# Kernel tuning notes

Measured on AMD Instinct MI355X. Metric: run time of the kernel, lower is better.

## Reference

```python
import jax, jax.numpy as jnp
import numpy as np

B, L, T = 8, 4096, 128
D_H, D_G, D_PROJ = 1024, 256, 256


def setup_inputs() -> dict:
    key = jax.random.key(0)
    k1, k2, k3, k4, k5 = jax.random.split(key, 5)
    H = jax.random.normal(k1, (B, L, D_H), dtype=jnp.float32)
    G = jax.random.normal(k2, (B, T, D_G), dtype=jnp.float32)
    mask = jax.random.randint(k3, (B, L), 0, 2) == 1  # True = masked out
    Wk = jax.random.normal(k4, (D_H, D_PROJ), dtype=jnp.float32) * 0.02
    Wq = jax.random.normal(k5, (D_G, D_PROJ), dtype=jnp.float32) * 0.02
    return {"H": H, "G": G, "mask": mask, "Wk": Wk, "Wq": Wq}


def reference(H, G, mask, Wk, Wq):
    scale = D_PROJ ** (-0.5)
    K = jnp.einsum('bld,dp->blp', H, Wk)          # [B, L, d_proj]
    Q = jnp.einsum('btd,dp->btp', G, Wq)          # [B, T, d_proj]
    logits = jnp.einsum('btp,blp->btl', Q, K) * scale  # [B, T, L]
    logits = jnp.where(mask[:, None, :], -jnp.inf, logits)
    alpha = jax.nn.softmax(logits, axis=-1)       # [B, T, L]
    Z = jnp.einsum('btl,bld->btd', alpha, H)      # [B, T, d_h]
    return Z
```

## Files before the change

kernel.cpp:

```cpp
#include <hip/hip_runtime.h>
#include <hip/hip_bf16.h>
#include <math.h>

#define B_  8
#define L_  4096
#define T_  128
#define DH  1024
#define DG  256
#define DP  256
#define BK  64
#define ZCH 8

typedef short bf16x8 __attribute__((ext_vector_type(8)));
typedef float f32x4  __attribute__((ext_vector_type(4)));
typedef unsigned short u16x8 __attribute__((ext_vector_type(8)));

#define AS1(p) ((const __attribute__((address_space(1))) void*)(p))
#define AS3(p) ((__attribute__((address_space(3))) void*)(p))

#define SYNC() do { asm volatile("s_waitcnt lgkmcnt(0)" ::: "memory"); \
                    __builtin_amdgcn_s_barrier(); \
                    __builtin_amdgcn_sched_barrier(0); } while (0)

__device__ __forceinline__ unsigned short f2bf(float f) {
    unsigned u = __float_as_uint(f);
    unsigned r = (u + 0x7FFFu + ((u >> 16) & 1u)) >> 16;
    return (unsigned short)r;
}

__device__ __forceinline__ char* swz(void* base, int row, int colbytes) {
    return (char*)base + (((row << 7) + colbytes) ^ ((row & 7) << 4));
}
__device__ __forceinline__ const char* swzc(const void* base, int row, int colbytes) {
    return (const char*)base + (((row << 7) + colbytes) ^ ((row & 7) << 4));
}

__global__ __launch_bounds__(256) void wct_kernel(const float* __restrict__ Wk,
                                                  const float* __restrict__ Wq,
                                                  unsigned short* __restrict__ Wct) {
    __shared__ __attribute__((aligned(16))) unsigned short As[128 * BK];
    __shared__ __attribute__((aligned(16))) unsigned short Bs[64 * BK];
    const int n0 = blockIdx.x * 64, m0 = blockIdx.y * 128;
    const int tid = threadIdx.x, wave = tid >> 6, lane = tid & 63;
    const int lm = lane & 15, quad = lane >> 4;
    const int wm = wave >> 1, wn = wave & 1;
    const int bc = (tid & 15) * 4, br = tid >> 4;
    f32x4 acc[4][2] = {};

    for (int k0 = 0; k0 < DP; k0 += BK) {
        #pragma unroll
        for (int s = 0; s < 8; ++s) {
            const int row = br + s * 16;
            const float4 v = *(const float4*)(Wk + (size_t)(m0 + row) * DP + k0 + bc);
            ushort4 p; p.x = f2bf(v.x); p.y = f2bf(v.y); p.z = f2bf(v.z); p.w = f2bf(v.w);
            *(ushort4*)(&As[row * BK + bc]) = p;
        }
        #pragma unroll
        for (int s = 0; s < 4; ++s) {
            const int row = br + s * 16;
            const float4 v = *(const float4*)(Wq + (size_t)(n0 + row) * DP + k0 + bc);
            ushort4 p; p.x = f2bf(v.x); p.y = f2bf(v.y); p.z = f2bf(v.z); p.w = f2bf(v.w);
            *(ushort4*)(&Bs[row * BK + bc]) = p;
        }
        __syncthreads();
        #pragma unroll
        for (int ks = 0; ks < 2; ++ks) {
            bf16x8 a[4], bf[2];
            #pragma unroll
            for (int i = 0; i < 4; ++i)
                a[i] = *(const bf16x8*)(&As[(wm * 64 + i * 16 + lm) * BK + ks * 32 + quad * 8]);
            #pragma unroll
            for (int j = 0; j < 2; ++j)
                bf[j] = *(const bf16x8*)(&Bs[(wn * 32 + j * 16 + lm) * BK + ks * 32 + quad * 8]);
            #pragma unroll
            for (int i = 0; i < 4; ++i)
                #pragma unroll
                for (int j = 0; j < 2; ++j)
                    acc[i][j] = __builtin_amdgcn_mfma_f32_16x16x32_bf16(a[i], bf[j], acc[i][j], 0, 0, 0);
        }
        __syncthreads();
    }
    unsigned short* Cb = Wct + (size_t)m0 * DG + n0;
    #pragma unroll
    for (int i = 0; i < 4; ++i)
        #pragma unroll
        for (int j = 0; j < 2; ++j)
            #pragma unroll
            for (int r = 0; r < 4; ++r)
                Cb[(size_t)(wm * 64 + i * 16 + quad * 4 + r) * DG + wn * 32 + j * 16 + lm] =
                    f2bf(acc[i][j][r] * 0.0625f);
}

__global__ __launch_bounds__(256) void qproj_kernel(const float* __restrict__ G,
                                                    const unsigned short* __restrict__ Wct,
                                                    unsigned short* __restrict__ Qk) {
    __shared__ __attribute__((aligned(16))) unsigned short As[128 * BK];
    __shared__ __attribute__((aligned(16))) unsigned short Bs[64 * BK];
    const int n0 = blockIdx.x * 64, m0 = blockIdx.y * 128;
    const int tid = threadIdx.x, wave = tid >> 6, lane = tid & 63;
    const int lm = lane & 15, quad = lane >> 4;
    const int wm = wave >> 1, wn = wave & 1;
    const int bc = (tid & 15) * 4, br = tid >> 4;
    const int ar = lane >> 3, akb = (lane & 7) * 8;
    f32x4 acc[4][2] = {};

    for (int k0 = 0; k0 < DG; k0 += BK) {
        #pragma unroll
        for (int s = 0; s < 8; ++s) {
            const int row = br + s * 16;
            const float4 v = *(const float4*)(G + (size_t)(m0 + row) * DG + k0 + bc);
            ushort4 p; p.x = f2bf(v.x); p.y = f2bf(v.y); p.z = f2bf(v.z); p.w = f2bf(v.w);
            *(ushort4*)(&As[row * BK + bc]) = p;
        }
        #pragma unroll
        for (int s = 0; s < 2; ++s) {
            const int rowb = s * 32 + wave * 8;
            const unsigned short* gp = Wct + (size_t)(n0 + rowb + ar) * DG + k0 + akb;
            __builtin_amdgcn_global_load_lds(AS1(gp), AS3(&Bs[rowb * BK]), 16, 0, 0);
        }
        __syncthreads();
        #pragma unroll
        for (int ks = 0; ks < 2; ++ks) {
            bf16x8 a[4], bf[2];
            #pragma unroll
            for (int i = 0; i < 4; ++i)
                a[i] = *(const bf16x8*)(&As[(wm * 64 + i * 16 + lm) * BK + ks * 32 + quad * 8]);
            #pragma unroll
            for (int j = 0; j < 2; ++j)
                bf[j] = *(const bf16x8*)(&Bs[(wn * 32 + j * 16 + lm) * BK + ks * 32 + quad * 8]);
            #pragma unroll
            for (int i = 0; i < 4; ++i)
                #pragma unroll
                for (int j = 0; j < 2; ++j)
                    acc[i][j] = __builtin_amdgcn_mfma_f32_16x16x32_bf16(a[i], bf[j], acc[i][j], 0, 0, 0);
        }
        __syncthreads();
    }
    unsigned short* Cb = Qk + (size_t)m0 * DH + n0;
    #pragma unroll
    for (int i = 0; i < 4; ++i)
        #pragma unroll
        for (int j = 0; j < 2; ++j)
            #pragma unroll
            for (int r = 0; r < 4; ++r)
                Cb[(size_t)(wm * 64 + i * 16 + quad * 4 + r) * DH + wn * 32 + j * 16 + lm] =
                    f2bf(acc[i][j][r]);
}

__global__ __launch_bounds__(256, 2) void fusedsm_kernel(const unsigned short* __restrict__ Qk,
                                                         const float* __restrict__ H,
                                                         const int* __restrict__ mask,
                                                         unsigned short* __restrict__ alpha,
                                                         float* __restrict__ rowsum,
                                                         unsigned short* __restrict__ H16) {
    __shared__ __attribute__((aligned(16))) unsigned short As[2][T_ * BK];
    __shared__ __attribute__((aligned(16))) unsigned short Bs[2][64 * BK];
    __shared__ float rs[T_];
    const int blin = blockIdx.x + (L_ / 64) * blockIdx.y;
    const int b = blin & 7, l0 = (blin >> 3) * 64;
    const int tid = threadIdx.x, wave = tid >> 6, lane = tid & 63;
    const unsigned short* Ab = Qk + (size_t)b * T_ * DH;
    const float*          Hb = H + ((size_t)b * L_ + l0) * DH;
    unsigned short*     H16b = H16 + ((size_t)b * L_ + l0) * DH;

    const int lm = lane & 15, quad = lane >> 4;
    const int wm = wave >> 1, wn = wave & 1;
    f32x4 acc[4][2] = {};
    const int ar = lane >> 3, akb = (lane & 7) * 8;
    const int bc = (tid & 15) * 4, br = tid >> 4;

    if (tid < T_) rs[tid] = 0.f;

    u16x8  qa0[4], qa1[4];
    float4 hv0[4], hv1[4];

    auto LOAD = [&](u16x8* qa, float4* hv, int kd) {
        #pragma unroll
        for (int s = 0; s < 4; ++s)
            qa[s] = *(const u16x8*)(Ab + (size_t)(s * 32 + wave * 8 + ar) * DH + kd + akb);
        #pragma unroll
        for (int s = 0; s < 4; ++s)
            hv[s] = *(const float4*)(Hb + (size_t)(br + s * 16) * DH + kd + bc);
    };
    auto WRITE = [&](int buf, const u16x8* qa, const float4* hv, int kd) {
        #pragma unroll
        for (int s = 0; s < 4; ++s)
            *(u16x8*)swz(&As[buf][0], s * 32 + wave * 8 + ar, akb * 2) = qa[s];
        #pragma unroll
        for (int s = 0; s < 4; ++s) {
            const int row = br + s * 16;
            ushort4 pk; pk.x = f2bf(hv[s].x); pk.y = f2bf(hv[s].y);
            pk.z = f2bf(hv[s].z); pk.w = f2bf(hv[s].w);
            *(ushort4*)swz(&Bs[buf][0], row, bc * 2) = pk;
            *(ushort4*)(H16b + (size_t)row * DH + kd + bc) = pk;
        }
    };
    auto COMPUTE = [&](int buf) {
        #pragma unroll
        for (int ks = 0; ks < 2; ++ks) {
            bf16x8 a[4], bfv[2];
            #pragma unroll
            for (int i = 0; i < 4; ++i) {
                const int row = wm * 64 + i * 16 + lm;
                a[i] = *(const bf16x8*)swzc(&As[buf][0], row, ks * 64 + quad * 16);
            }
            #pragma unroll
            for (int j = 0; j < 2; ++j) {
                const int row = wn * 32 + j * 16 + lm;
                bfv[j] = *(const bf16x8*)swzc(&Bs[buf][0], row, ks * 64 + quad * 16);
            }
            #pragma unroll
            for (int i = 0; i < 4; ++i)
                #pragma unroll
                for (int j = 0; j < 2; ++j)
                    acc[i][j] = __builtin_amdgcn_mfma_f32_16x16x32_bf16(a[i], bfv[j], acc[i][j], 0, 0, 0);
        }
    };

    const int nT = DH / BK;
    LOAD(qa0, hv0, 0);
    LOAD(qa1, hv1, BK);
    WRITE(0, qa0, hv0, 0);
    SYNC();

    for (int tt = 0; tt < nT; tt += 2) {
        if (tt + 2 < nT) LOAD(qa0, hv0, (tt + 2) * BK);
        COMPUTE(0);
        WRITE(1, qa1, hv1, (tt + 1) * BK);
        SYNC();
        if (tt + 3 < nT) LOAD(qa1, hv1, (tt + 3) * BK);
        COMPUTE(1);
        if (tt + 2 < nT) WRITE(0, qa0, hv0, (tt + 2) * BK);
        SYNC();
    }

    const int c0 = l0 + wn * 32 + lm;
    const int mk0 = mask[(size_t)b * L_ + c0];
    const int mk1 = mask[(size_t)b * L_ + c0 + 16];
    unsigned short* Arow = alpha + (size_t)b * T_ * L_ + l0 + wn * 32 + lm;
    #pragma unroll
    for (int i = 0; i < 4; ++i) {
        #pragma unroll
        for (int r = 0; r < 4; ++r) {
            const int row = wm * 64 + i * 16 + quad * 4 + r;
            float e0 = mk0 ? 0.f : __expf(acc[i][0][r]);
            float e1 = mk1 ? 0.f : __expf(acc[i][1][r]);
            Arow[(size_t)row * L_]      = f2bf(e0);
            Arow[(size_t)row * L_ + 16] = f2bf(e1);
            float part = e0 + e1;
            part += __shfl_xor(part, 1, 64);
            part += __shfl_xor(part, 2, 64);
            part += __shfl_xor(part, 4, 64);
            part += __shfl_xor(part, 8, 64);
            if (lm == 0) atomicAdd(&rs[row], part);
        }
    }
    __syncthreads();
    if (tid < T_) atomicAdd(&rowsum[(size_t)b * T_ + tid], rs[tid]);
}

__global__ __launch_bounds__(256, 2) void z_kernel(const unsigned short* __restrict__ alpha,
                                                   const unsigned short* __restrict__ H16,
                                                   float* __restrict__ part) {
    __shared__ __attribute__((aligned(16))) unsigned short As[2][T_ * BK];
    __shared__ __attribute__((aligned(16))) unsigned B32[2][128 * 32];
    const int blin = blockIdx.x + 8 * (blockIdx.y + 8 * blockIdx.z);
    const int ch = blin & 7, rest = blin >> 3;
    const int b = rest & 7, d0 = (rest >> 3) * 128;
    const int tid = threadIdx.x, wave = tid >> 6, lane = tid & 63;
    const int Lc = L_ / ZCH;
    const unsigned short* Ab = alpha + (size_t)b * T_ * L_ + ch * Lc;
    const unsigned short* Hb = H16 + ((size_t)b * L_ + ch * Lc) * DH + d0;

    const int lm = lane & 15, quad = lane >> 4;
    const int wm = wave >> 1, wn = wave & 1;
    f32x4 acc[4][4] = {};
    const int ar = lane >> 3, akb = (lane & 7) * 8;
    const int dg = tid & 15, lph = tid >> 4;
    const int lp0 = 2 * lph;

    u16x8 qa0[4], qa1[4];
    u16x8 hu0[4], hu1[4];

    auto LOAD = [&](u16x8* qa, u16x8* hu, int kd) {
        #pragma unroll
        for (int s = 0; s < 4; ++s)
            qa[s] = *(const u16x8*)(Ab + (size_t)(s * 32 + wave * 8 + ar) * L_ + kd + akb);
        const unsigned short* r = Hb + (size_t)(kd + 4 * lph) * DH + dg * 8;
        #pragma unroll
        for (int rr = 0; rr < 4; ++rr)
            hu[rr] = *(const u16x8*)(r + (size_t)rr * DH);
    };
    auto WRITE = [&](int buf, const u16x8* qa, const u16x8* hu) {
        #pragma unroll
        for (int s = 0; s < 4; ++s)
            *(u16x8*)swz(&As[buf][0], s * 32 + wave * 8 + ar, akb * 2) = qa[s];
        #pragma unroll
        for (int i = 0; i < 8; ++i) {
            const int d   = dg * 8 + i;
            const int rot = ((i + (dg & 7)) << 2) & 31;
            B32[buf][d * 32 + ((lp0 + rot) & 31)]     = (unsigned)hu[0][i] | ((unsigned)hu[1][i] << 16);
            B32[buf][d * 32 + ((lp0 + 1 + rot) & 31)] = (unsigned)hu[2][i] | ((unsigned)hu[3][i] << 16);
        }
    };
    auto COMPUTE = [&](int buf) {
        #pragma unroll
        for (int ks = 0; ks < 2; ++ks) {
            bf16x8 a[4], bfv[4];
            #pragma unroll
            for (int i = 0; i < 4; ++i) {
                const int row = wm * 64 + i * 16 + lm;
                a[i] = *(const bf16x8*)swzc(&As[buf][0], row, ks * 64 + quad * 16);
            }
            #pragma unroll
            for (int j = 0; j < 4; ++j) {
                const int d   = wn * 64 + j * 16 + lm;
                const int rot = (((d & 7) + ((d >> 3) & 7)) << 2) & 31;
                bfv[j] = *(const bf16x8*)(&B32[buf][d * 32 + ((ks * 16 + quad * 4 + rot) & 31)]);
            }
            #pragma unroll
            for (int i = 0; i < 4; ++i)
                #pragma unroll
                for (int j = 0; j < 4; ++j)
                    acc[i][j] = __builtin_amdgcn_mfma_f32_16x16x32_bf16(a[i], bfv[j], acc[i][j], 0, 0, 0);
        }
    };

    const int nT = Lc / BK;
    LOAD(qa0, hu0, 0);
    LOAD(qa1, hu1, BK);
    WRITE(0, qa0, hu0);
    SYNC();

    for (int tt = 0; tt < nT; tt += 2) {
        if (tt + 2 < nT) LOAD(qa0, hu0, (tt + 2) * BK);
        COMPUTE(0);
        WRITE(1, qa1, hu1);
        SYNC();
        if (tt + 3 < nT) LOAD(qa1, hu1, (tt + 3) * BK);
        COMPUTE(1);
        if (tt + 2 < nT) WRITE(0, qa0, hu0);
        SYNC();
    }

    float* Cb = part + (((size_t)ch * B_ + b) * T_) * DH + d0;
    #pragma unroll
    for (int i = 0; i < 4; ++i)
        #pragma unroll
        for (int j = 0; j < 4; ++j)
            #pragma unroll
            for (int r = 0; r < 4; ++r)
                Cb[(size_t)(wm * 64 + i * 16 + quad * 4 + r) * DH + wn * 64 + j * 16 + lm] = acc[i][j][r];
}

__global__ __launch_bounds__(256) void zreduce_kernel(const float* __restrict__ p,
                                                      const float* __restrict__ rowsum,
                                                      float* __restrict__ Z) {
    const size_t n = (size_t)B_ * T_ * DH;
    const size_t i = ((size_t)blockIdx.x * 256 + threadIdx.x) * 4;
    const int row = (int)(i >> 10);
    const float inv = 1.0f / rowsum[row];
    float4 o = {0.f, 0.f, 0.f, 0.f};
    #pragma unroll
    for (int c = 0; c < ZCH; ++c) {
        const float4 a = *(const float4*)(p + (size_t)c * n + i);
        o.x += a.x; o.y += a.y; o.z += a.z; o.w += a.w;
    }
    o.x *= inv; o.y *= inv; o.z *= inv; o.w *= inv;
    *(float4*)(Z + i) = o;
}

extern "C" void kernel_launch(void* const* d_in, const int* in_sizes, int n_in,
                              void* d_out, int out_size, void* d_ws, size_t ws_size,
                              hipStream_t stream) {
    const float* H    = (const float*)d_in[0];
    const float* G    = (const float*)d_in[1];
    const int*   mask = (const int*)d_in[2];
    const float* Wk   = (const float*)d_in[3];
    const float* Wq   = (const float*)d_in[4];
    float* Z = (float*)d_out;

    char* ws = (char*)d_ws;
    unsigned short* Wct    = (unsigned short*)ws;
    unsigned short* Qk     = (unsigned short*)(ws + ((size_t)1 << 20));
    unsigned short* alpha  = (unsigned short*)(ws + ((size_t)4 << 20));
    float*          rowsum = (float*)(ws + ((size_t)13 << 20));
    unsigned short* H16    = (unsigned short*)(ws + ((size_t)14 << 20));
    float*          zpart  = (float*)(ws + ((size_t)80 << 20));

    hipMemsetAsync(rowsum, 0, (size_t)B_ * T_ * sizeof(float), stream);
    wct_kernel<<<dim3(DG / 64, DH / 128), 256, 0, stream>>>(Wk, Wq, Wct);
    qproj_kernel<<<dim3(DH / 64, (B_ * T_) / 128), 256, 0, stream>>>(G, Wct, Qk);
    fusedsm_kernel<<<dim3(L_ / 64, B_), 256, 0, stream>>>(Qk, H, mask, alpha, rowsum, H16);
    z_kernel<<<dim3(DH / 128, B_, ZCH), 256, 0, stream>>>(alpha, H16, zpart);
    zreduce_kernel<<<(B_ * T_ * DH / 4) / 256, 256, 0, stream>>>(zpart, rowsum, Z);
}
```

Before: 282.9 us.

## Split fused softmax and Z kernels into smaller tiles for more blocks

The fused logits/softmax kernel now splits the T dimension into two 64-row halves per block, doubling the grid to 1024 blocks with smaller accumulators. Only one half writes the bf16 copy of H. The Z kernel halves its D tile to 64 columns, also giving 1024 blocks, and raises its occupancy hint. The aim is more concurrent blocks and better latency hiding on the many CUs. The cost is that each fp32 H tile is now read and converted twice in the fused kernel, and alpha is re-read more times in the Z kernel.

```diff
diff --git a/kernel.cpp b/kernel.cpp
--- a/kernel.cpp
+++ b/kernel.cpp
@@ -147,70 +147,68 @@
                     f2bf(acc[i][j][r]);
 }
 
-__global__ __launch_bounds__(256, 2) void fusedsm_kernel(const unsigned short* __restrict__ Qk,
+__global__ __launch_bounds__(256, 4) void fusedsm_kernel(const unsigned short* __restrict__ Qk,
                                                          const float* __restrict__ H,
                                                          const int* __restrict__ mask,
                                                          unsigned short* __restrict__ alpha,
                                                          float* __restrict__ rowsum,
                                                          unsigned short* __restrict__ H16) {
-    __shared__ __attribute__((aligned(16))) unsigned short As[2][T_ * BK];
+    __shared__ __attribute__((aligned(16))) unsigned short As[2][64 * BK];
     __shared__ __attribute__((aligned(16))) unsigned short Bs[2][64 * BK];
-    __shared__ float rs[T_];
-    const int blin = blockIdx.x + (L_ / 64) * blockIdx.y;
-    const int b = blin & 7, l0 = (blin >> 3) * 64;
+    __shared__ float rs[64];
+    const int blin = blockIdx.x;
+    const int b = blin & 7, rem = blin >> 3;
+    const int l0 = (rem >> 1) * 64, t0 = (rem & 1) * 64;
     const int tid = threadIdx.x, wave = tid >> 6, lane = tid & 63;
-    const unsigned short* Ab = Qk + (size_t)b * T_ * DH;
+    const unsigned short* Ab = Qk + ((size_t)b * T_ + t0) * DH;
     const float*          Hb = H + ((size_t)b * L_ + l0) * DH;
     unsigned short*     H16b = H16 + ((size_t)b * L_ + l0) * DH;
+    const bool doSpill = (t0 == 0);
 
     const int lm = lane & 15, quad = lane >> 4;
     const int wm = wave >> 1, wn = wave & 1;
-    f32x4 acc[4][2] = {};
-    const int ar = lane >> 3, akb = (lane & 7) * 8;
+    f32x4 acc[2][2] = {};
+    const int ar2 = tid >> 3, ag8 = (tid & 7) * 8;
     const int bc = (tid & 15) * 4, br = tid >> 4;
 
-    if (tid < T_) rs[tid] = 0.f;
-
-    u16x8  qa0[4], qa1[4];
+    if (tid < 64) rs[tid] = 0.f;
+
+    u16x8  qa0[2], qa1[2];
     float4 hv0[4], hv1[4];
 
     auto LOAD = [&](u16x8* qa, float4* hv, int kd) {
         #pragma unroll
-        for (int s = 0; s < 4; ++s)
-            qa[s] = *(const u16x8*)(Ab + (size_t)(s * 32 + wave * 8 + ar) * DH + kd + akb);
+        for (int s = 0; s < 2; ++s)
+            qa[s] = *(const u16x8*)(Ab + (size_t)(s * 32 + ar2) * DH + kd + ag8);
         #pragma unroll
         for (int s = 0; s < 4; ++s)
             hv[s] = *(const float4*)(Hb + (size_t)(br + s * 16) * DH + kd + bc);
     };
     auto WRITE = [&](int buf, const u16x8* qa, const float4* hv, int kd) {
         #pragma unroll
-        for (int s = 0; s < 4; ++s)
-            *(u16x8*)swz(&As[buf][0], s * 32 + wave * 8 + ar, akb * 2) = qa[s];
+        for (int s = 0; s < 2; ++s)
+            *(u16x8*)swz(&As[buf][0], s * 32 + ar2, ag8 * 2) = qa[s];
         #pragma unroll
         for (int s = 0; s < 4; ++s) {
             const int row = br + s * 16;
             ushort4 pk; pk.x = f2bf(hv[s].x); pk.y = f2bf(hv[s].y);
             pk.z = f2bf(hv[s].z); pk.w = f2bf(hv[s].w);
             *(ushort4*)swz(&Bs[buf][0], row, bc * 2) = pk;
-            *(ushort4*)(H16b + (size_t)row * DH + kd + bc) = pk;
+            if (doSpill) *(ushort4*)(H16b + (size_t)row * DH + kd + bc) = pk;
         }
     };
     auto COMPUTE = [&](int buf) {
         #pragma unroll
         for (int ks = 0; ks < 2; ++ks) {
-            bf16x8 a[4], bfv[2];
-            #pragma unroll
-            for (int i = 0; i < 4; ++i) {
-                const int row = wm * 64 + i * 16 + lm;
-                a[i] = *(const bf16x8*)swzc(&As[buf][0], row, ks * 64 + quad * 16);
-            }
-            #pragma unroll
-            for (int j = 0; j < 2; ++j) {
-                const int row = wn * 32 + j * 16 + lm;
-                bfv[j] = *(const bf16x8*)swzc(&Bs[buf][0], row, ks * 64 + quad * 16);
-            }
-            #pragma unroll
-            for (int i = 0; i < 4; ++i)
+            bf16x8 a[2], bfv[2];
+            #pragma unroll
+            for (int i = 0; i < 2; ++i)
+                a[i] = *(const bf16x8*)swzc(&As[buf][0], wm * 32 + i * 16 + lm, ks * 64 + quad * 16);
+            #pragma unroll
+            for (int j = 0; j < 2; ++j)
+                bfv[j] = *(const bf16x8*)swzc(&Bs[buf][0], wn * 32 + j * 16 + lm, ks * 64 + quad * 16);
+            #pragma unroll
+            for (int i = 0; i < 2; ++i)
                 #pragma unroll
                 for (int j = 0; j < 2; ++j)
                     acc[i][j] = __builtin_amdgcn_mfma_f32_16x16x32_bf16(a[i], bfv[j], acc[i][j], 0, 0, 0);
@@ -237,12 +235,12 @@
     const int c0 = l0 + wn * 32 + lm;
     const int mk0 = mask[(size_t)b * L_ + c0];
     const int mk1 = mask[(size_t)b * L_ + c0 + 16];
-    unsigned short* Arow = alpha + (size_t)b * T_ * L_ + l0 + wn * 32 + lm;
-    #pragma unroll
-    for (int i = 0; i < 4; ++i) {
+    unsigned short* Arow = alpha + ((size_t)b * T_ + t0) * L_ + l0 + wn * 32 + lm;
+    #pragma unroll
+    for (int i = 0; i < 2; ++i) {
         #pragma unroll
         for (int r = 0; r < 4; ++r) {
-            const int row = wm * 64 + i * 16 + quad * 4 + r;
+            const int row = wm * 32 + i * 16 + quad * 4 + r;
             float e0 = mk0 ? 0.f : __expf(acc[i][0][r]);
             float e1 = mk1 ? 0.f : __expf(acc[i][1][r]);
             Arow[(size_t)row * L_]      = f2bf(e0);
@@ -256,17 +254,17 @@
         }
     }
     __syncthreads();
-    if (tid < T_) atomicAdd(&rowsum[(size_t)b * T_ + tid], rs[tid]);
-}
-
-__global__ __launch_bounds__(256, 2) void z_kernel(const unsigned short* __restrict__ alpha,
+    if (tid < 64) atomicAdd(&rowsum[(size_t)b * T_ + t0 + tid], rs[tid]);
+}
+
+__global__ __launch_bounds__(256, 3) void z_kernel(const unsigned short* __restrict__ alpha,
                                                    const unsigned short* __restrict__ H16,
                                                    float* __restrict__ part) {
     __shared__ __attribute__((aligned(16))) unsigned short As[2][T_ * BK];
-    __shared__ __attribute__((aligned(16))) unsigned B32[2][128 * 32];
-    const int blin = blockIdx.x + 8 * (blockIdx.y + 8 * blockIdx.z);
-    const int ch = blin & 7, rest = blin >> 3;
-    const int b = rest & 7, d0 = (rest >> 3) * 128;
+    __shared__ __attribute__((aligned(16))) unsigned B32[2][64 * 32];
+    const int blin = blockIdx.x;
+    const int ch = blin & 7, rem = blin >> 3;
+    const int b = rem & 7, d0 = (rem >> 3) * 64;
     const int tid = threadIdx.x, wave = tid >> 6, lane = tid & 63;
     const int Lc = L_ / ZCH;
     const unsigned short* Ab = alpha + (size_t)b * T_ * L_ + ch * Lc;
@@ -274,54 +272,48 @@
 
     const int lm = lane & 15, quad = lane >> 4;
     const int wm = wave >> 1, wn = wave & 1;
-    f32x4 acc[4][4] = {};
-    const int ar = lane >> 3, akb = (lane & 7) * 8;
-    const int dg = tid & 15, lph = tid >> 4;
-    const int lp0 = 2 * lph;
+    f32x4 acc[4][2] = {};
+    const int a_r = tid >> 3, a_g = (tid & 7) * 8;
+    const int dg = tid & 7, lph = tid >> 3;
 
     u16x8 qa0[4], qa1[4];
-    u16x8 hu0[4], hu1[4];
+    u16x8 hu0[2], hu1[2];
 
     auto LOAD = [&](u16x8* qa, u16x8* hu, int kd) {
         #pragma unroll
         for (int s = 0; s < 4; ++s)
-            qa[s] = *(const u16x8*)(Ab + (size_t)(s * 32 + wave * 8 + ar) * L_ + kd + akb);
-        const unsigned short* r = Hb + (size_t)(kd + 4 * lph) * DH + dg * 8;
-        #pragma unroll
-        for (int rr = 0; rr < 4; ++rr)
-            hu[rr] = *(const u16x8*)(r + (size_t)rr * DH);
+            qa[s] = *(const u16x8*)(Ab + (size_t)(s * 32 + a_r) * L_ + kd + a_g);
+        hu[0] = *(const u16x8*)(Hb + (size_t)(kd + 2 * lph) * DH + dg * 8);
+        hu[1] = *(const u16x8*)(Hb + (size_t)(kd + 2 * lph + 1) * DH + dg * 8);
     };
     auto WRITE = [&](int buf, const u16x8* qa, const u16x8* hu) {
         #pragma unroll
         for (int s = 0; s < 4; ++s)
-            *(u16x8*)swz(&As[buf][0], s * 32 + wave * 8 + ar, akb * 2) = qa[s];
+            *(u16x8*)swz(&As[buf][0], s * 32 + a_r, a_g * 2) = qa[s];
         #pragma unroll
         for (int i = 0; i < 8; ++i) {
             const int d   = dg * 8 + i;
-            const int rot = ((i + (dg & 7)) << 2) & 31;
-            B32[buf][d * 32 + ((lp0 + rot) & 31)]     = (unsigned)hu[0][i] | ((unsigned)hu[1][i] << 16);
-            B32[buf][d * 32 + ((lp0 + 1 + rot) & 31)] = (unsigned)hu[2][i] | ((unsigned)hu[3][i] << 16);
+            const int rot = ((i + dg) << 2) & 31;
+            B32[buf][d * 32 + ((lph + rot) & 31)] = (unsigned)hu[0][i] | ((unsigned)hu[1][i] << 16);
         }
     };
     auto COMPUTE = [&](int buf) {
         #pragma unroll
         for (int ks = 0; ks < 2; ++ks) {
-            bf16x8 a[4], bfv[4];
-            #pragma unroll
-            for (int i = 0; i < 4; ++i) {
-                const int row = wm * 64 + i * 16 + lm;
-                a[i] = *(const bf16x8*)swzc(&As[buf][0], row, ks * 64 + quad * 16);
-            }
-            #pragma unroll
-            for (int j = 0; j < 4; ++j) {
-                const int d   = wn * 64 + j * 16 + lm;
+            bf16x8 a[4], bfv[2];
+            #pragma unroll
+            for (int i = 0; i < 4; ++i)
+                a[i] = *(const bf16x8*)swzc(&As[buf][0], wm * 64 + i * 16 + lm, ks * 64 + quad * 16);
+            #pragma unroll
+            for (int j = 0; j < 2; ++j) {
+                const int d   = wn * 32 + j * 16 + lm;
                 const int rot = (((d & 7) + ((d >> 3) & 7)) << 2) & 31;
                 bfv[j] = *(const bf16x8*)(&B32[buf][d * 32 + ((ks * 16 + quad * 4 + rot) & 31)]);
             }
             #pragma unroll
             for (int i = 0; i < 4; ++i)
                 #pragma unroll
-                for (int j = 0; j < 4; ++j)
+                for (int j = 0; j < 2; ++j)
                     acc[i][j] = __builtin_amdgcn_mfma_f32_16x16x32_bf16(a[i], bfv[j], acc[i][j], 0, 0, 0);
         }
     };
@@ -347,10 +339,10 @@
     #pragma unroll
     for (int i = 0; i < 4; ++i)
         #pragma unroll
-        for (int j = 0; j < 4; ++j)
+        for (int j = 0; j < 2; ++j)
             #pragma unroll
             for (int r = 0; r < 4; ++r)
-                Cb[(size_t)(wm * 64 + i * 16 + quad * 4 + r) * DH + wn * 64 + j * 16 + lm] = acc[i][j][r];
+                Cb[(size_t)(wm * 64 + i * 16 + quad * 4 + r) * DH + wn * 32 + j * 16 + lm] = acc[i][j][r];
 }
 
 __global__ __launch_bounds__(256) void zreduce_kernel(const float* __restrict__ p,
@@ -391,7 +383,7 @@
     hipMemsetAsync(rowsum, 0, (size_t)B_ * T_ * sizeof(float), stream);
     wct_kernel<<<dim3(DG / 64, DH / 128), 256, 0, stream>>>(Wk, Wq, Wct);
     qproj_kernel<<<dim3(DH / 64, (B_ * T_) / 128), 256, 0, stream>>>(G, Wct, Qk);
-    fusedsm_kernel<<<dim3(L_ / 64, B_), 256, 0, stream>>>(Qk, H, mask, alpha, rowsum, H16);
-    z_kernel<<<dim3(DH / 128, B_, ZCH), 256, 0, stream>>>(alpha, H16, zpart);
+    fusedsm_kernel<<<1024, 256, 0, stream>>>(Qk, H, mask, alpha, rowsum, H16);
+    z_kernel<<<1024, 256, 0, stream>>>(alpha, H16, zpart);
     zreduce_kernel<<<(B_ * T_ * DH / 4) / 256, 256, 0, stream>>>(zpart, rowsum, Z);
 }
```

Measured after the change: 284.4 us. No clear change (+0.6%).
